# Optimization experiments

Measured on AMD Instinct MI355X. Metric: run time of the kernel, lower is better.

The kernel has to match this reference:

```python
import jax, jax.numpy as jnp
import numpy as np

FEATURE_HEIGHT = 50
FEATURE_WIDTH = 50


def setup_inputs() -> dict:
    key = jax.random.key(0)
    k1, k2, k3 = jax.random.split(key, 3)
    bs, K, H, D = 16, FEATURE_HEIGHT * FEATURE_WIDTH, 8, 32
    Q, L, P = 2000, 1, 4
    value = jax.random.normal(k1, (bs, K, H, D), dtype=jnp.float32)
    value_spatial_shapes = jnp.array([[FEATURE_HEIGHT, FEATURE_WIDTH]], dtype=jnp.int64)
    sampling_locations = jax.random.uniform(k2, (bs, Q, H, L, P, 2), dtype=jnp.float32)
    attention_weights = jax.random.uniform(k3, (bs, Q, H, L, P), dtype=jnp.float32)
    return {
        "value": value,
        "value_spatial_shapes": value_spatial_shapes,
        "sampling_locations": sampling_locations,
        "attention_weights": attention_weights,
    }


def _bilinear_sample(img, grid):
    """torch.F.grid_sample(mode='bilinear', padding_mode='zeros', align_corners=False).

    img:  (N, D, h, w)
    grid: (N, Q, P, 2), last dim (x, y) in [-1, 1]
    returns (N, D, Q, P)
    """
    N, D, h, w = img.shape
    # unnormalize (align_corners=False)
    x = (grid[..., 0] + 1.0) * (w * 0.5) - 0.5  # (N, Q, P)
    y = (grid[..., 1] + 1.0) * (h * 0.5) - 0.5
    x0 = jnp.floor(x)
    y0 = jnp.floor(y)
    x1 = x0 + 1.0
    y1 = y0 + 1.0
    wx1 = x - x0
    wx0 = 1.0 - wx1
    wy1 = y - y0
    wy0 = 1.0 - wy1

    img_flat = img.reshape(N, D, h * w)

    def corner(ix, iy, wgt):
        valid = ((ix >= 0) & (ix < w) & (iy >= 0) & (iy < h)).astype(img.dtype)
        ixc = jnp.clip(ix, 0, w - 1).astype(jnp.int32)
        iyc = jnp.clip(iy, 0, h - 1).astype(jnp.int32)
        idx = (iyc * w + ixc).reshape(N, -1)  # (N, Q*P)
        vals = jnp.take_along_axis(img_flat, idx[:, None, :], axis=2)  # (N, D, Q*P)
        vals = vals.reshape(N, D, *ix.shape[1:])  # (N, D, Q, P)
        return vals * (wgt * valid)[:, None]

    out = corner(x0, y0, wx0 * wy0)
    out = out + corner(x1, y0, wx1 * wy0)
    out = out + corner(x0, y1, wx0 * wy1)
    out = out + corner(x1, y1, wx1 * wy1)
    return out


def reference(value, value_spatial_shapes, sampling_locations, attention_weights):
    bs, K, H, D = value.shape
    _, Q, _, L, P, _ = sampling_locations.shape
    h, w = FEATURE_HEIGHT, FEATURE_WIDTH

    sampling_grids = 2.0 * sampling_locations - 1.0  # (bs, Q, H, L, P, 2)
    # value -> (bs*H, D, h, w)
    v = value.reshape(bs, K, H * D).transpose(0, 2, 1).reshape(bs * H, D, h, w)
    # level 0 grid -> (bs*H, Q, P, 2)
    g = jnp.transpose(sampling_grids[:, :, :, 0], (0, 2, 1, 3, 4)).reshape(bs * H, Q, P, 2)
    sampled = _bilinear_sample(v, g)  # (bs*H, D, Q, P)
    # attention weights -> (bs*H, 1, Q, L*P)
    aw = jnp.transpose(attention_weights, (0, 2, 1, 3, 4)).reshape(bs * H, 1, Q, L * P)
    out = (sampled * aw).sum(-1)  # (bs*H, D, Q)
    out = out.reshape(bs, H * D, Q).transpose(0, 2, 1)  # (bs, Q, H*D)
    return out
```

## Files before the change

### kernel.cpp

```cpp
#include <hip/hip_runtime.h>


#define FH 50
#define FW 50
#define KK (FH * FW)
#define NH 8
#define ND 32
#define NQ 2000
#define NP 4

#define QPB 4
#define BLOCKS_PER_B (NQ / QPB)

__global__ __launch_bounds__(256) void deform_attn_kernel(
    const float* __restrict__ value,
    const float* __restrict__ loc,
    const float* __restrict__ attw,
    float* __restrict__ out)
{
    const int x = blockIdx.x;
    const int xcd = x & 7;
    const int slot = x >> 3;
    const int phase = (slot >= BLOCKS_PER_B) ? 1 : 0;
    const int b = xcd + (phase << 3);
    const int q0 = (slot - phase * BLOCKS_PER_B) * QPB;

    const int lg = threadIdx.x >> 3;
    const int c = threadIdx.x & 7;
    const int h = lg & (NH - 1);
    const int q = q0 + (lg >> 3);
    const int bq = b * NQ + q;
    const int gid = bq * NH + h;

    const float4* __restrict__ vbase =
        (const float4*)value + ((size_t)b * KK * NH + (size_t)h) * (ND / 4) + c;

    const float4* __restrict__ locp = (const float4*)loc + (size_t)gid * 2;
    const float4 lv0 = locp[0];
    const float4 lv1 = locp[1];
    const float4 aw4 = ((const float4*)attw)[gid];

    const float px[NP] = {lv0.x, lv0.z, lv1.x, lv1.z};
    const float py[NP] = {lv0.y, lv0.w, lv1.y, lv1.w};
    const float aw[NP] = {aw4.x, aw4.y, aw4.z, aw4.w};

    float4 acc = {0.f, 0.f, 0.f, 0.f};
#pragma unroll
    for (int p = 0; p < NP; ++p) {
        const float fx = px[p] * (float)FW - 0.5f;
        const float fy = py[p] * (float)FH - 0.5f;
        const float x0f = floorf(fx);
        const float y0f = floorf(fy);
        const int x0 = (int)x0f, y0 = (int)y0f;
        const int x1 = x0 + 1, y1 = y0 + 1;
        const float wx1 = fx - x0f, wx0 = 1.f - wx1;
        const float wy1 = fy - y0f, wy0 = 1.f - wy1;

        const bool vx0 = (x0 >= 0) && (x0 < FW);
        const bool vx1 = (x1 >= 0) && (x1 < FW);
        const bool vy0 = (y0 >= 0) && (y0 < FH);
        const bool vy1 = (y1 >= 0) && (y1 < FH);

        const int cx0 = min(max(x0, 0), FW - 1);
        const int cx1 = min(max(x1, 0), FW - 1);
        const int cy0 = min(max(y0, 0), FH - 1);
        const int cy1 = min(max(y1, 0), FH - 1);

        const float4 v00 = vbase[(size_t)(cy0 * FW + cx0) * (NH * ND / 4)];
        const float4 v10 = vbase[(size_t)(cy0 * FW + cx1) * (NH * ND / 4)];
        const float4 v01 = vbase[(size_t)(cy1 * FW + cx0) * (NH * ND / 4)];
        const float4 v11 = vbase[(size_t)(cy1 * FW + cx1) * (NH * ND / 4)];

        const float w00 = ((vx0 && vy0) ? (wx0 * wy0) : 0.f) * aw[p];
        const float w10 = ((vx1 && vy0) ? (wx1 * wy0) : 0.f) * aw[p];
        const float w01 = ((vx0 && vy1) ? (wx0 * wy1) : 0.f) * aw[p];
        const float w11 = ((vx1 && vy1) ? (wx1 * wy1) : 0.f) * aw[p];

        acc.x += w00 * v00.x + w10 * v10.x + w01 * v01.x + w11 * v11.x;
        acc.y += w00 * v00.y + w10 * v10.y + w01 * v01.y + w11 * v11.y;
        acc.z += w00 * v00.z + w10 * v10.z + w01 * v01.z + w11 * v11.z;
        acc.w += w00 * v00.w + w10 * v10.w + w01 * v01.w + w11 * v11.w;
    }

    ((float4*)out)[(size_t)bq * (NH * ND / 4) + h * (ND / 4) + c] = acc;
}

extern "C" void kernel_launch(void* const* d_in, const int* in_sizes, int n_in,
                              void* d_out, int out_size, void* d_ws, size_t ws_size,
                              hipStream_t stream) {
    const float* value = (const float*)d_in[0];
    const float* loc  = (const float*)d_in[2];
    const float* attw = (const float*)d_in[3];
    float* out = (float*)d_out;

    const int blocks = 16 * BLOCKS_PER_B;
    deform_attn_kernel<<<blocks, 256, 0, stream>>>(value, loc, attw, out);
}
```

Before: 119.4 us.

## Process two queries per thread with batched gathers and 32-bit byte offsets

Each block now covers 8 queries instead of 4, so every thread handles two (query, head) pairs and the grid is half as large. Within each pair, all 16 corner offsets and weights are computed first and then all 16 float4 gathers are issued before any accumulation, which exposes more memory-level parallelism. Addressing switches to 32-bit byte offsets from a per-batch base pointer, and launch bounds add a minimum of two blocks per CU. The cost is higher register pressure and fewer blocks, which could lower occupancy or tail efficiency.

```diff
diff --git a/kernel.cpp b/kernel.cpp
--- a/kernel.cpp
+++ b/kernel.cpp
@@ -9,10 +9,10 @@
 #define NQ 2000
 #define NP 4
 
-#define QPB 4
+#define QPB 8
 #define BLOCKS_PER_B (NQ / QPB)
 
-__global__ __launch_bounds__(256) void deform_attn_kernel(
+__global__ __launch_bounds__(256, 2) void deform_attn_kernel(
     const float* __restrict__ value,
     const float* __restrict__ loc,
     const float* __restrict__ attw,
@@ -25,64 +25,85 @@
     const int b = xcd + (phase << 3);
     const int q0 = (slot - phase * BLOCKS_PER_B) * QPB;
 
-    const int lg = threadIdx.x >> 3;
-    const int c = threadIdx.x & 7;
-    const int h = lg & (NH - 1);
-    const int q = q0 + (lg >> 3);
-    const int bq = b * NQ + q;
-    const int gid = bq * NH + h;
+    const int t = threadIdx.x;
+    const int c = t & 7;
+    const int lg = t >> 3;
+    const int h = lg & 7;
+    const int qo = lg >> 3;
 
-    const float4* __restrict__ vbase =
-        (const float4*)value + ((size_t)b * KK * NH + (size_t)h) * (ND / 4) + c;
+    const char* __restrict__ vb =
+        (const char*)(value + (size_t)b * KK * NH * ND);
+    const int hc = h * (ND * 4) + c * 16;
 
-    const float4* __restrict__ locp = (const float4*)loc + (size_t)gid * 2;
-    const float4 lv0 = locp[0];
-    const float4 lv1 = locp[1];
-    const float4 aw4 = ((const float4*)attw)[gid];
+    const int qA = q0 + qo;
+    const int gidA = (b * NQ + qA) * NH + h;
 
-    const float px[NP] = {lv0.x, lv0.z, lv1.x, lv1.z};
-    const float py[NP] = {lv0.y, lv0.w, lv1.y, lv1.w};
-    const float aw[NP] = {aw4.x, aw4.y, aw4.z, aw4.w};
+    float4 accA = {0.f, 0.f, 0.f, 0.f};
+    float4 accB = {0.f, 0.f, 0.f, 0.f};
 
-    float4 acc = {0.f, 0.f, 0.f, 0.f};
+    auto sample = [&](int gid, float4& acc) {
+        const float4* __restrict__ lp = (const float4*)loc + (size_t)gid * 2;
+        const float4 l0 = lp[0];
+        const float4 l1 = lp[1];
+        const float4 a4 = ((const float4*)attw)[gid];
+
+        const float pxx[NP] = {l0.x, l0.z, l1.x, l1.z};
+        const float pyy[NP] = {l0.y, l0.w, l1.y, l1.w};
+        const float awp[NP] = {a4.x, a4.y, a4.z, a4.w};
+
+        unsigned offs[16];
+        float wts[16];
 #pragma unroll
-    for (int p = 0; p < NP; ++p) {
-        const float fx = px[p] * (float)FW - 0.5f;
-        const float fy = py[p] * (float)FH - 0.5f;
-        const float x0f = floorf(fx);
-        const float y0f = floorf(fy);
-        const int x0 = (int)x0f, y0 = (int)y0f;
-        const int x1 = x0 + 1, y1 = y0 + 1;
-        const float wx1 = fx - x0f, wx0 = 1.f - wx1;
-        const float wy1 = fy - y0f, wy0 = 1.f - wy1;
+        for (int p = 0; p < NP; ++p) {
+            const float fx = pxx[p] * (float)FW - 0.5f;
+            const float fy = pyy[p] * (float)FH - 0.5f;
+            const float x0f = floorf(fx);
+            const float y0f = floorf(fy);
+            const int x0 = (int)x0f, y0 = (int)y0f;
+            const int x1 = x0 + 1, y1 = y0 + 1;
+            const float wx1 = fx - x0f, wx0 = 1.f - wx1;
+            const float wy1 = fy - y0f, wy0 = 1.f - wy1;
 
-        const bool vx0 = (x0 >= 0) && (x0 < FW);
-        const bool vx1 = (x1 >= 0) && (x1 < FW);
-        const bool vy0 = (y0 >= 0) && (y0 < FH);
-        const bool vy1 = (y1 >= 0) && (y1 < FH);
+            const bool vx0 = (x0 >= 0) & (x0 < FW);
+            const bool vx1 = (x1 >= 0) & (x1 < FW);
+            const bool vy0 = (y0 >= 0) & (y0 < FH);
+            const bool vy1 = (y1 >= 0) & (y1 < FH);
 
-        const int cx0 = min(max(x0, 0), FW - 1);
-        const int cx1 = min(max(x1, 0), FW - 1);
-        const int cy0 = min(max(y0, 0), FH - 1);
-        const int cy1 = min(max(y1, 0), FH - 1);
+            const int cx0 = min(max(x0, 0), FW - 1);
+            const int cx1 = min(max(x1, 0), FW - 1);
+            const int cy0 = min(max(y0, 0), FH - 1);
+            const int cy1 = min(max(y1, 0), FH - 1);
 
-        const float4 v00 = vbase[(size_t)(cy0 * FW + cx0) * (NH * ND / 4)];
-        const float4 v10 = vbase[(size_t)(cy0 * FW + cx1) * (NH * ND / 4)];
-        const float4 v01 = vbase[(size_t)(cy1 * FW + cx0) * (NH * ND / 4)];
-        const float4 v11 = vbase[(size_t)(cy1 * FW + cx1) * (NH * ND / 4)];
+            offs[p * 4 + 0] = (unsigned)((cy0 * FW + cx0) * 1024 + hc);
+            offs[p * 4 + 1] = (unsigned)((cy0 * FW + cx1) * 1024 + hc);
+            offs[p * 4 + 2] = (unsigned)((cy1 * FW + cx0) * 1024 + hc);
+            offs[p * 4 + 3] = (unsigned)((cy1 * FW + cx1) * 1024 + hc);
 
-        const float w00 = ((vx0 && vy0) ? (wx0 * wy0) : 0.f) * aw[p];
-        const float w10 = ((vx1 && vy0) ? (wx1 * wy0) : 0.f) * aw[p];
-        const float w01 = ((vx0 && vy1) ? (wx0 * wy1) : 0.f) * aw[p];
-        const float w11 = ((vx1 && vy1) ? (wx1 * wy1) : 0.f) * aw[p];
+            wts[p * 4 + 0] = ((vx0 & vy0) ? (wx0 * wy0) : 0.f) * awp[p];
+            wts[p * 4 + 1] = ((vx1 & vy0) ? (wx1 * wy0) : 0.f) * awp[p];
+            wts[p * 4 + 2] = ((vx0 & vy1) ? (wx0 * wy1) : 0.f) * awp[p];
+            wts[p * 4 + 3] = ((vx1 & vy1) ? (wx1 * wy1) : 0.f) * awp[p];
+        }
 
-        acc.x += w00 * v00.x + w10 * v10.x + w01 * v01.x + w11 * v11.x;
-        acc.y += w00 * v00.y + w10 * v10.y + w01 * v01.y + w11 * v11.y;
-        acc.z += w00 * v00.z + w10 * v10.z + w01 * v01.z + w11 * v11.z;
-        acc.w += w00 * v00.w + w10 * v10.w + w01 * v01.w + w11 * v11.w;
-    }
+        float4 v[16];
+#pragma unroll
+        for (int i = 0; i < 16; ++i)
+            v[i] = *(const float4*)(vb + offs[i]);
+#pragma unroll
+        for (int i = 0; i < 16; ++i) {
+            acc.x += wts[i] * v[i].x;
+            acc.y += wts[i] * v[i].y;
+            acc.z += wts[i] * v[i].z;
+            acc.w += wts[i] * v[i].w;
+        }
+    };
 
-    ((float4*)out)[(size_t)bq * (NH * ND / 4) + h * (ND / 4) + c] = acc;
+    sample(gidA, accA);
+    sample(gidA + 4 * NH, accB);
+
+    float4* __restrict__ op = (float4*)out;
+    op[(size_t)(b * NQ + qA) * (NH * ND / 4) + h * (ND / 4) + c] = accA;
+    op[(size_t)(b * NQ + qA + 4) * (NH * ND / 4) + h * (ND / 4) + c] = accB;
 }
 
 extern "C" void kernel_launch(void* const* d_in, const int* in_sizes, int n_in,
```

Result: no change. 118.3 us (-0.9%).
